# Kernel tuning notes

Measured on AMD Instinct MI355X. Metric: run time of the kernel, lower is better.

Reference implementation:

```python
import jax, jax.numpy as jnp
import numpy as np

B, F = 1048576, 128


def setup_inputs() -> dict:
    key = jax.random.key(0)
    ks = jax.random.split(key, 16)
    def w(k, shape):
        return jax.random.normal(k, shape, dtype=jnp.float32) * 0.1
    x = jax.random.uniform(ks[0], (B, F), dtype=jnp.float32, minval=0.05, maxval=1.0)
    return {
        "x": x,
        "W_prod": w(ks[1], (F, 1)), "b_prod": w(ks[2], (1,)),
        "W_sum": w(ks[3], (F + 1, 1)), "b_sum": w(ks[4], (1,)),
        "w_dln": w(ks[5], (1, 1)), "W_ln": w(ks[6], (2, 1)),
        "w_dsin": w(ks[7], (1, 1)), "W_sin": w(ks[8], (2, 1)),
        "w_dcos": w(ks[9], (1, 1)), "W_cos": w(ks[10], (2, 1)),
        "w_de": w(ks[11], (1, 1)), "W_e": w(ks[12], (2, 1)),
        "w_dtanh": w(ks[13], (1, 1)), "W_tanh": w(ks[14], (2, 1)),
    }


def _stage(h, fn, w_drop, W):
    # h: [B,1]. Drop = Dense(1, relu, no bias) on fn(h); then Dense(2->1, no bias)
    d = jax.nn.relu(fn(h) * w_drop[0, 0])          # [B,1]
    return jnp.concatenate([d, h], axis=-1) @ W    # [B,1]


def reference(x, W_prod, b_prod, W_sum, b_sum,
              w_dln, W_ln, w_dsin, W_sin, w_dcos, W_cos,
              w_de, W_e, w_dtanh, W_tanh):
    # ProductBlock: exp(Dense(log(abs(x))))  -> product-of-powers via log-space
    x_prod = jnp.exp(jnp.log(jnp.abs(x)) @ W_prod + b_prod)          # [B,1]
    # SumBlock over [x, x_prod]
    x_sum = jnp.concatenate([x, x_prod], axis=-1) @ W_sum + b_sum    # [B,1]
    x_ln = _stage(x_sum, lambda t: jnp.log(jnp.abs(t)), w_dln, W_ln)
    x_sin = _stage(x_ln, jnp.sin, w_dsin, W_sin)
    x_cos = _stage(x_sin, jnp.cos, w_dcos, W_cos)
    x_e = _stage(x_cos, jnp.exp, w_de, W_e)
    x_tanh = _stage(x_e, jnp.tanh, w_dtanh, W_tanh)
    return x_tanh
```

## Files before the change

### kernel.cpp

```cpp
#include <hip/hip_runtime.h>


__global__ __launch_bounds__(256) void funcblock_kernel(
    const float* __restrict__ x,
    const float* __restrict__ W_prod, const float* __restrict__ b_prod,
    const float* __restrict__ W_sum,  const float* __restrict__ b_sum,
    const float* __restrict__ w_dln,  const float* __restrict__ W_ln,
    const float* __restrict__ w_dsin, const float* __restrict__ W_sin,
    const float* __restrict__ w_dcos, const float* __restrict__ W_cos,
    const float* __restrict__ w_de,   const float* __restrict__ W_e,
    const float* __restrict__ w_dtanh,const float* __restrict__ W_tanh,
    float* __restrict__ out, int B)
{
    const int tid  = threadIdx.x;
    const int lane = tid & 63;
    const int wid  = tid >> 6;
    const int u    = lane & 7;
    const int g    = lane >> 3;

    float4 wp[4], ws[4];
    #pragma unroll
    for (int j = 0; j < 4; ++j) {
        wp[j] = reinterpret_cast<const float4*>(W_prod)[u + 8 * j];
        ws[j] = reinterpret_cast<const float4*>(W_sum)[u + 8 * j];
    }
    const float ws128 = W_sum[128];
    const float bp2 = b_prod[0] * 1.44269504088896340736f;
    const float bs = b_sum[0];
    const float wdln  = w_dln[0],  wln0  = W_ln[0],  wln1  = W_ln[1];
    const float wdsin = w_dsin[0], wsin0 = W_sin[0], wsin1 = W_sin[1];
    const float wdcos = w_dcos[0], wcos0 = W_cos[0], wcos1 = W_cos[1];
    const float wde   = w_de[0],   we0   = W_e[0],   we1   = W_e[1];
    const float wdtanh= w_dtanh[0],wt0   = W_tanh[0],wt1   = W_tanh[1];

    const int wbase = (blockIdx.x * 4 + wid) * 64;

    float pr = 0.0f, sr = 0.0f;
    #pragma unroll 4
    for (int it = 0; it < 8; ++it) {
        const int row = wbase + it * 8 + g;
        float p = 0.0f, s = 0.0f;
        if (row < B) {
            const float4* xr =
                reinterpret_cast<const float4*>(x + (size_t)row * 128);
            float4 xv[4];
            #pragma unroll
            for (int j = 0; j < 4; ++j) xv[j] = xr[u + 8 * j];
            #pragma unroll
            for (int j = 0; j < 4; ++j) {
                p += __log2f(__builtin_fabsf(xv[j].x)) * wp[j].x;
                p += __log2f(__builtin_fabsf(xv[j].y)) * wp[j].y;
                p += __log2f(__builtin_fabsf(xv[j].z)) * wp[j].z;
                p += __log2f(__builtin_fabsf(xv[j].w)) * wp[j].w;
                s += xv[j].x * ws[j].x + xv[j].y * ws[j].y
                   + xv[j].z * ws[j].z + xv[j].w * ws[j].w;
            }
        }
        #pragma unroll
        for (int m = 4; m >= 1; m >>= 1) {
            p += __shfl_xor(p, m, 64);
            s += __shfl_xor(s, m, 64);
        }
        const float pb = __shfl(p, (lane & 7) * 8, 64);
        const float sb = __shfl(s, (lane & 7) * 8, 64);
        if (g == it) { pr = pb; sr = sb; }
    }

    const float x_prod = __builtin_amdgcn_exp2f(pr + bp2);
    float h = sr + x_prod * ws128 + bs;
    float d;
    d = fmaxf(logf(fabsf(h)) * wdln, 0.0f);  h = d * wln0  + h * wln1;
    d = fmaxf(sinf(h) * wdsin, 0.0f);        h = d * wsin0 + h * wsin1;
    d = fmaxf(cosf(h) * wdcos, 0.0f);        h = d * wcos0 + h * wcos1;
    d = fmaxf(expf(h) * wde,   0.0f);        h = d * we0   + h * we1;
    d = fmaxf(tanhf(h) * wdtanh, 0.0f);      h = d * wt0   + h * wt1;
    const int orow = wbase + lane;
    if (orow < B) out[orow] = h;
}

extern "C" void kernel_launch(void* const* d_in, const int* in_sizes, int n_in,
                              void* d_out, int out_size, void* d_ws, size_t ws_size,
                              hipStream_t stream) {
    const float* x      = (const float*)d_in[0];
    const float* W_prod = (const float*)d_in[1];
    const float* b_prod = (const float*)d_in[2];
    const float* W_sum  = (const float*)d_in[3];
    const float* b_sum  = (const float*)d_in[4];
    const float* w_dln  = (const float*)d_in[5];
    const float* W_ln   = (const float*)d_in[6];
    const float* w_dsin = (const float*)d_in[7];
    const float* W_sin  = (const float*)d_in[8];
    const float* w_dcos = (const float*)d_in[9];
    const float* W_cos  = (const float*)d_in[10];
    const float* w_de   = (const float*)d_in[11];
    const float* W_e    = (const float*)d_in[12];
    const float* w_dtanh= (const float*)d_in[13];
    const float* W_tanh = (const float*)d_in[14];
    float* out = (float*)d_out;

    const int B = out_size;
    const int block = 256;
    const int grid  = (B + 255) / 256;

    hipLaunchKernelGGL(funcblock_kernel, dim3(grid), dim3(block), 0, stream,
                       x, W_prod, b_prod, W_sum, b_sum,
                       w_dln, W_ln, w_dsin, W_sin, w_dcos, W_cos,
                       w_de, W_e, w_dtanh, W_tanh, out, B);
}
```

Measured before the change: 101.5 us.

## Split fused kernel into dot-product kernel and scalar chain kernel via workspace

```diff
diff --git a/kernel.cpp b/kernel.cpp
--- a/kernel.cpp
+++ b/kernel.cpp
@@ -1,7 +1,84 @@
 #include <hip/hip_runtime.h>
 
 
-__global__ __launch_bounds__(256) void funcblock_kernel(
+__global__ __launch_bounds__(256) void dot_kernel(
+    const float* __restrict__ x,
+    const float* __restrict__ W_prod,
+    const float* __restrict__ W_sum,
+    float2* __restrict__ ps)
+{
+    const int tid  = threadIdx.x;
+    const int lane = tid & 63;
+    const int wid  = tid >> 6;
+    const int u    = lane & 7;
+    const int g    = lane >> 3;
+
+    float4 wp[4], ws[4];
+    #pragma unroll
+    for (int j = 0; j < 4; ++j) {
+        wp[j] = reinterpret_cast<const float4*>(W_prod)[u + 8 * j];
+        ws[j] = reinterpret_cast<const float4*>(W_sum)[u + 8 * j];
+    }
+
+    const int wbase = (blockIdx.x * 4 + wid) * 64;
+
+    float pr = 0.0f, sr = 0.0f;
+    #pragma unroll
+    for (int it = 0; it < 8; ++it) {
+        const int row = wbase + it * 8 + g;
+        const float4* xr = reinterpret_cast<const float4*>(x + (size_t)row * 128);
+        float4 xv[4];
+        #pragma unroll
+        for (int j = 0; j < 4; ++j) xv[j] = xr[u + 8 * j];
+        float p = 0.0f, s = 0.0f;
+        #pragma unroll
+        for (int j = 0; j < 4; ++j) {
+            p += __log2f(__builtin_fabsf(xv[j].x)) * wp[j].x;
+            p += __log2f(__builtin_fabsf(xv[j].y)) * wp[j].y;
+            p += __log2f(__builtin_fabsf(xv[j].z)) * wp[j].z;
+            p += __log2f(__builtin_fabsf(xv[j].w)) * wp[j].w;
+            s += xv[j].x * ws[j].x + xv[j].y * ws[j].y
+               + xv[j].z * ws[j].z + xv[j].w * ws[j].w;
+        }
+        #pragma unroll
+        for (int m = 4; m >= 1; m >>= 1) {
+            p += __shfl_xor(p, m, 64);
+            s += __shfl_xor(s, m, 64);
+        }
+        const float pb = __shfl(p, (lane & 7) * 8, 64);
+        const float sb = __shfl(s, (lane & 7) * 8, 64);
+        if (g == it) { pr = pb; sr = sb; }
+    }
+    ps[wbase + lane] = make_float2(pr, sr);
+}
+
+__global__ __launch_bounds__(256) void chain_kernel(
+    const float2* __restrict__ ps,
+    const float* __restrict__ b_prod, const float* __restrict__ W_sum,
+    const float* __restrict__ b_sum,
+    const float* __restrict__ w_dln,  const float* __restrict__ W_ln,
+    const float* __restrict__ w_dsin, const float* __restrict__ W_sin,
+    const float* __restrict__ w_dcos, const float* __restrict__ W_cos,
+    const float* __restrict__ w_de,   const float* __restrict__ W_e,
+    const float* __restrict__ w_dtanh,const float* __restrict__ W_tanh,
+    float* __restrict__ out, int B)
+{
+    const int i = blockIdx.x * 256 + threadIdx.x;
+    if (i >= B) return;
+    const float2 v = ps[i];
+    const float bp2 = b_prod[0] * 1.44269504088896340736f;
+    const float x_prod = __builtin_amdgcn_exp2f(v.x + bp2);
+    float h = v.y + x_prod * W_sum[128] + b_sum[0];
+    float d;
+    d = fmaxf(logf(fabsf(h)) * w_dln[0], 0.0f);   h = d * W_ln[0]   + h * W_ln[1];
+    d = fmaxf(sinf(h) * w_dsin[0], 0.0f);         h = d * W_sin[0]  + h * W_sin[1];
+    d = fmaxf(cosf(h) * w_dcos[0], 0.0f);         h = d * W_cos[0]  + h * W_cos[1];
+    d = fmaxf(expf(h) * w_de[0],   0.0f);         h = d * W_e[0]    + h * W_e[1];
+    d = fmaxf(tanhf(h) * w_dtanh[0], 0.0f);       h = d * W_tanh[0] + h * W_tanh[1];
+    out[i] = h;
+}
+
+__global__ __launch_bounds__(256) void fused_kernel(
     const float* __restrict__ x,
     const float* __restrict__ W_prod, const float* __restrict__ b_prod,
     const float* __restrict__ W_sum,  const float* __restrict__ b_sum,
@@ -17,7 +94,6 @@
     const int wid  = tid >> 6;
     const int u    = lane & 7;
     const int g    = lane >> 3;
-
     float4 wp[4], ws[4];
     #pragma unroll
     for (int j = 0; j < 4; ++j) {
@@ -27,22 +103,14 @@
     const float ws128 = W_sum[128];
     const float bp2 = b_prod[0] * 1.44269504088896340736f;
     const float bs = b_sum[0];
-    const float wdln  = w_dln[0],  wln0  = W_ln[0],  wln1  = W_ln[1];
-    const float wdsin = w_dsin[0], wsin0 = W_sin[0], wsin1 = W_sin[1];
-    const float wdcos = w_dcos[0], wcos0 = W_cos[0], wcos1 = W_cos[1];
-    const float wde   = w_de[0],   we0   = W_e[0],   we1   = W_e[1];
-    const float wdtanh= w_dtanh[0],wt0   = W_tanh[0],wt1   = W_tanh[1];
-
     const int wbase = (blockIdx.x * 4 + wid) * 64;
-
     float pr = 0.0f, sr = 0.0f;
     #pragma unroll 4
     for (int it = 0; it < 8; ++it) {
         const int row = wbase + it * 8 + g;
         float p = 0.0f, s = 0.0f;
         if (row < B) {
-            const float4* xr =
-                reinterpret_cast<const float4*>(x + (size_t)row * 128);
+            const float4* xr = reinterpret_cast<const float4*>(x + (size_t)row * 128);
             float4 xv[4];
             #pragma unroll
             for (int j = 0; j < 4; ++j) xv[j] = xr[u + 8 * j];
@@ -65,15 +133,14 @@
         const float sb = __shfl(s, (lane & 7) * 8, 64);
         if (g == it) { pr = pb; sr = sb; }
     }
-
     const float x_prod = __builtin_amdgcn_exp2f(pr + bp2);
     float h = sr + x_prod * ws128 + bs;
     float d;
-    d = fmaxf(logf(fabsf(h)) * wdln, 0.0f);  h = d * wln0  + h * wln1;
-    d = fmaxf(sinf(h) * wdsin, 0.0f);        h = d * wsin0 + h * wsin1;
-    d = fmaxf(cosf(h) * wdcos, 0.0f);        h = d * wcos0 + h * wcos1;
-    d = fmaxf(expf(h) * wde,   0.0f);        h = d * we0   + h * we1;
-    d = fmaxf(tanhf(h) * wdtanh, 0.0f);      h = d * wt0   + h * wt1;
+    d = fmaxf(logf(fabsf(h)) * w_dln[0], 0.0f);   h = d * W_ln[0]   + h * W_ln[1];
+    d = fmaxf(sinf(h) * w_dsin[0], 0.0f);         h = d * W_sin[0]  + h * W_sin[1];
+    d = fmaxf(cosf(h) * w_dcos[0], 0.0f);         h = d * W_cos[0]  + h * W_cos[1];
+    d = fmaxf(expf(h) * w_de[0],   0.0f);         h = d * W_e[0]    + h * W_e[1];
+    d = fmaxf(tanhf(h) * w_dtanh[0], 0.0f);       h = d * W_tanh[0] + h * W_tanh[1];
     const int orow = wbase + lane;
     if (orow < B) out[orow] = h;
 }
@@ -99,11 +166,20 @@
     float* out = (float*)d_out;
 
     const int B = out_size;
-    const int block = 256;
-    const int grid  = (B + 255) / 256;
+    const bool split_ok = (ws_size >= (size_t)B * sizeof(float2)) && (B % 256 == 0);
 
-    hipLaunchKernelGGL(funcblock_kernel, dim3(grid), dim3(block), 0, stream,
-                       x, W_prod, b_prod, W_sum, b_sum,
-                       w_dln, W_ln, w_dsin, W_sin, w_dcos, W_cos,
-                       w_de, W_e, w_dtanh, W_tanh, out, B);
+    if (split_ok) {
+        float2* ps = (float2*)d_ws;
+        hipLaunchKernelGGL(dot_kernel, dim3(B / 256), dim3(256), 0, stream,
+                           x, W_prod, W_sum, ps);
+        hipLaunchKernelGGL(chain_kernel, dim3(B / 256), dim3(256), 0, stream,
+                           ps, b_prod, W_sum, b_sum,
+                           w_dln, W_ln, w_dsin, W_sin, w_dcos, W_cos,
+                           w_de, W_e, w_dtanh, W_tanh, out, B);
+    } else {
+        hipLaunchKernelGGL(fused_kernel, dim3((B + 255) / 256), dim3(256), 0, stream,
+                           x, W_prod, b_prod, W_sum, b_sum,
+                           w_dln, W_ln, w_dsin, W_sin, w_dcos, W_cos,
+                           w_de, W_e, w_dtanh, W_tanh, out, B);
+    }
 }
```

Measured after the change: 109.4 us. +7.7%, slower.
